# Optimization experiments

Hardware: AMD Instinct MI355X
Metric: run time of the kernel (lower is better)

## Reference

```python
import jax, jax.numpy as jnp
import numpy as np

N, D, H = 4096, 1024, 8
HD = D // H
FFN = int(D * 1.5)
TAU_NEG = 0.6
BETA = 1.5
LN_EPS = 1e-5


def _layernorm(x, g, b):
    mu = jnp.mean(x, axis=-1, keepdims=True)
    var = jnp.mean((x - mu) ** 2, axis=-1, keepdims=True)
    return (x - mu) * jax.lax.rsqrt(var + LN_EPS) * g + b


def setup_inputs() -> dict:
    key = jax.random.key(0)
    ks = jax.random.split(key, 16)
    s = 0.02
    inp = {
        "features": jax.random.normal(ks[0], (N, D), jnp.float32),
        "coords": jax.random.randint(ks[1], (N, 2), 0, 128, jnp.int32),
        "Wq": jax.random.normal(ks[2], (D, D), jnp.float32) * s,
        "Wk": jax.random.normal(ks[3], (D, D), jnp.float32) * s,
        "Wv": jax.random.normal(ks[4], (D, D), jnp.float32) * s,
        "Wo": jax.random.normal(ks[5], (D, D), jnp.float32) * s,
        "bo": jnp.zeros((D,), jnp.float32),
        "ln1_g": jnp.ones((D,), jnp.float32),
        "ln1_b": jnp.zeros((D,), jnp.float32),
        "W1": jax.random.normal(ks[6], (FFN, D), jnp.float32) * s,
        "b1": jnp.zeros((FFN,), jnp.float32),
        "W2": jax.random.normal(ks[7], (D, FFN), jnp.float32) * s,
        "b2": jnp.zeros((D,), jnp.float32),
        "ln2_g": jnp.ones((D,), jnp.float32),
        "ln2_b": jnp.zeros((D,), jnp.float32),
    }
    return inp


def reference(features, coords, Wq, Wk, Wv, Wo, bo, ln1_g, ln1_b, W1, b1, W2, b2, ln2_g, ln2_b):
    # QKV projections (torch Linear: x @ W.T), reshape to [H, N, HD]
    Q = (features @ Wq.T).reshape(N, H, HD).transpose(1, 0, 2)
    K = (features @ Wk.T).reshape(N, H, HD).transpose(1, 0, 2)
    V = (features @ Wv.T).reshape(N, H, HD).transpose(1, 0, 2)

    scores = jnp.einsum('hnd,hmd->hnm', Q, K) / jnp.sqrt(jnp.float32(HD))  # [H,N,N]

    # spatial distance bias from barcode coords, scaled per head by 1/2^(h+1)
    c = coords.astype(jnp.float32)
    diff = c[:, None, :] - c[None, :, :]
    dist = jnp.sqrt(jnp.sum(diff ** 2, axis=-1))  # [N,N]
    head_scalings = 1.0 / (2.0 ** (jnp.arange(1, H + 1, dtype=jnp.float32)))
    bias = dist[None, :, :] * head_scalings[:, None, None]  # [H,N,N]

    attn_pos = jax.nn.softmax(scores - bias, axis=-1)
    attn_neg = jax.nn.softmax((-scores - bias) / TAU_NEG, axis=-1)
    attn = attn_pos - BETA * attn_neg  # dropout is identity in eval

    attended = jnp.einsum('hnm,hmd->hnd', attn, V)  # [H,N,HD]
    attended = attended.transpose(1, 0, 2).reshape(N, D)

    x = attended @ Wo.T + bo + features
    x = _layernorm(x, ln1_g, ln1_b)

    h = jax.nn.gelu(x @ W1.T + b1, approximate=False)  # torch default GELU = exact erf
    ffn_out = h @ W2.T + b2
    return _layernorm(ffn_out + x, ln2_g, ln2_b)
```

## Files before the change

kernel.cpp:

```cpp
#include <hip/hip_runtime.h>
#include <cstdint>
#include <cstddef>

#define NTOK 4096
#define DMODEL 1024
#define NHEAD 8
#define DHEAD 128
#define DFFN 1536
#define LNEPS 1e-5f

typedef __bf16 bf16_t;
typedef __bf16 bf16x8 __attribute__((ext_vector_type(8)));
typedef __bf16 bf16x4 __attribute__((ext_vector_type(4)));
typedef float f32x4 __attribute__((ext_vector_type(4)));
typedef float f32x16 __attribute__((ext_vector_type(16)));

__device__ __forceinline__ void gload_lds16(const bf16_t* g, bf16_t* lds) {
  __builtin_amdgcn_global_load_lds(
      (const __attribute__((address_space(1))) unsigned int*)g,
      (__attribute__((address_space(3))) unsigned int*)lds, 16, 0, 0);
}

__device__ __forceinline__ float fexp2(float x) {
  float r;
  asm("v_exp_f32 %0, %1" : "=v"(r) : "v"(x));
  return r;
}
__device__ __forceinline__ float fsqrt(float x) {
  float r;
  asm("v_sqrt_f32 %0, %1" : "=v"(r) : "v"(x));
  return r;
}
__device__ __forceinline__ unsigned cvtpk(float lo, float hi) {
  unsigned r;
  asm("v_cvt_pk_bf16_f32 %0, %1, %2" : "=v"(r) : "v"(lo), "v"(hi));
  return r;
}

#define CVT_TOTAL 2885632
__global__ __launch_bounds__(256) void cvt_all(
    const float* __restrict__ f, const float* __restrict__ wq,
    const float* __restrict__ wk, const float* __restrict__ wv,
    const float* __restrict__ wo, const float* __restrict__ w1,
    const float* __restrict__ w2, const int* __restrict__ coords,
    bf16_t* __restrict__ fb, bf16_t* __restrict__ wqkv,
    bf16_t* __restrict__ wob, bf16_t* __restrict__ w1b,
    bf16_t* __restrict__ w2b, float2* __restrict__ cfl)
{
  for (int u = blockIdx.x * 256 + threadIdx.x; u < CVT_TOTAL; u += 2048 * 256) {
    if (u < 2048) {
      int4 c = reinterpret_cast<const int4*>(coords)[u];
      float4 o;
      o.x = (float)c.x; o.y = (float)c.y; o.z = (float)c.z; o.w = (float)c.w;
      reinterpret_cast<float4*>(cfl)[u] = o;
      continue;
    }
    int v = u - 2048;
    const float* src; bf16_t* dst; int base;
    if (v < 1048576)      { src = f;  dst = fb;            base = 0; }
    else if (v < 1310720) { src = wq; dst = wqkv;          base = 1048576; }
    else if (v < 1572864) { src = wk; dst = wqkv + 1048576; base = 1310720; }
    else if (v < 1835008) { src = wv; dst = wqkv + 2097152; base = 1572864; }
    else if (v < 2097152) { src = wo; dst = wob;           base = 1835008; }
    else if (v < 2490368) { src = w1; dst = w1b;           base = 2097152; }
    else                  { src = w2; dst = w2b;           base = 2490368; }
    int local = v - base;
    const float4 x = reinterpret_cast<const float4*>(src)[local];
    bf16x4 o = {(bf16_t)x.x, (bf16_t)x.y, (bf16_t)x.z, (bf16_t)x.w};
    reinterpret_cast<bf16x4*>(dst)[local] = o;
  }
}

template<int EPI>
__global__ __launch_bounds__(256) void gemm_bt(
    const bf16_t* __restrict__ A, const bf16_t* __restrict__ B,
    int M, int Nn, int K,
    const float* __restrict__ bias, const float* __restrict__ resid,
    const bf16_t* __restrict__ residH,
    float* __restrict__ outF, bf16_t* __restrict__ outH)
{
  __shared__ bf16_t As[2][64 * 32];
  __shared__ bf16_t Bs[2][128 * 32];
  const int t = threadIdx.x;
  const int w = t >> 6, l = t & 63;
  const int lg = l >> 4, li = l & 15;
  const int m0 = blockIdx.x * 64, n0 = blockIdx.y * 128;
  const int wr = (w >> 1) * 32, wc = (w & 1) * 64;
  const f32x4 fz = {0.f, 0.f, 0.f, 0.f};
  f32x4 acc[2][4];
#pragma unroll
  for (int i = 0; i < 2; i++)
#pragma unroll
    for (int j = 0; j < 4; j++) acc[i][j] = fz;

  const bf16_t* Ag = A + (size_t)m0 * K;
  const bf16_t* Bg = B + (size_t)n0 * K;
  const int ca = w * 64 + l;
  const int nK = K >> 5;

  gload_lds16(Ag + (size_t)(ca >> 2) * K + (ca & 3) * 8, &As[0][(w * 64) * 8]);
#pragma unroll
  for (int p = 0; p < 2; p++) {
    int cb = p * 256 + ca;
    gload_lds16(Bg + (size_t)(cb >> 2) * K + (cb & 3) * 8, &Bs[0][(p * 256 + w * 64) * 8]);
  }
  __syncthreads();

  for (int ki = 0; ki < nK; ki++) {
    const int cur = ki & 1;
    if (ki + 1 < nK) {
      const int kt = (ki + 1) << 5;
      gload_lds16(Ag + (size_t)(ca >> 2) * K + kt + (ca & 3) * 8,
                  &As[cur ^ 1][(w * 64) * 8]);
#pragma unroll
      for (int p = 0; p < 2; p++) {
        int cb = p * 256 + ca;
        gload_lds16(Bg + (size_t)(cb >> 2) * K + kt + (cb & 3) * 8,
                    &Bs[cur ^ 1][(p * 256 + w * 64) * 8]);
      }
    }
    bf16x8 af[2], bfr[4];
#pragma unroll
    for (int mi = 0; mi < 2; mi++)
      af[mi] = *reinterpret_cast<const bf16x8*>(&As[cur][(wr + mi * 16 + li) * 32 + lg * 8]);
#pragma unroll
    for (int ni = 0; ni < 4; ni++)
      bfr[ni] = *reinterpret_cast<const bf16x8*>(&Bs[cur][(wc + ni * 16 + li) * 32 + lg * 8]);
#pragma unroll
    for (int mi = 0; mi < 2; mi++)
#pragma unroll
      for (int ni = 0; ni < 4; ni++)
        acc[mi][ni] = __builtin_amdgcn_mfma_f32_16x16x32_bf16(af[mi], bfr[ni], acc[mi][ni], 0, 0, 0);
    __syncthreads();
  }

#pragma unroll
  for (int mi = 0; mi < 2; mi++) {
#pragma unroll
    for (int ni = 0; ni < 4; ni++) {
      int gcol = n0 + wc + ni * 16 + li;
#pragma unroll
      for (int r = 0; r < 4; r++) {
        int grow = m0 + wr + mi * 16 + lg * 4 + r;
        float v = acc[mi][ni][r];
        if (EPI == 0) {
          outH[(size_t)grow * Nn + gcol] = (bf16_t)v;
        } else if (EPI == 1) {
          v += bias[gcol] + resid[(size_t)grow * Nn + gcol];
          outF[(size_t)grow * Nn + gcol] = v;
        } else if (EPI == 2) {
          v += bias[gcol];
          v = 0.5f * v * (1.f + erff(v * 0.70710678118654752f));
          outH[(size_t)grow * Nn + gcol] = (bf16_t)v;
        } else {
          v += bias[gcol] + (float)residH[(size_t)grow * Nn + gcol];
          outF[(size_t)grow * Nn + gcol] = v;
        }
      }
    }
  }
}

__global__ __launch_bounds__(256) void gemm_qkv(
    const bf16_t* __restrict__ A, const bf16_t* __restrict__ B,
    bf16_t* __restrict__ Qo, bf16_t* __restrict__ Kp, bf16_t* __restrict__ Vp)
{
  const int K = DMODEL;
  __shared__ bf16_t As[2][64 * 32];
  __shared__ bf16_t Bs[2][128 * 32];
  const int t = threadIdx.x;
  const int w = t >> 6, l = t & 63;
  const int lg = l >> 4, li = l & 15;
  const int m0 = blockIdx.x * 64, n0 = blockIdx.y * 128;
  const int wr = (w >> 1) * 32, wc = (w & 1) * 64;
  const f32x4 fz = {0.f, 0.f, 0.f, 0.f};
  f32x4 acc[2][4];
#pragma unroll
  for (int i = 0; i < 2; i++)
#pragma unroll
    for (int j = 0; j < 4; j++) acc[i][j] = fz;

  const bf16_t* Ag = A + (size_t)m0 * K;
  const bf16_t* Bg = B + (size_t)n0 * K;
  const int ca = w * 64 + l;
  const int nK = K >> 5;

  gload_lds16(Ag + (size_t)(ca >> 2) * K + (ca & 3) * 8, &As[0][(w * 64) * 8]);
#pragma unroll
  for (int p = 0; p < 2; p++) {
    int cb = p * 256 + ca;
    gload_lds16(Bg + (size_t)(cb >> 2) * K + (cb & 3) * 8, &Bs[0][(p * 256 + w * 64) * 8]);
  }
  __syncthreads();

  for (int ki = 0; ki < nK; ki++) {
    const int cur = ki & 1;
    if (ki + 1 < nK) {
      const int kt = (ki + 1) << 5;
      gload_lds16(Ag + (size_t)(ca >> 2) * K + kt + (ca & 3) * 8,
                  &As[cur ^ 1][(w * 64) * 8]);
#pragma unroll
      for (int p = 0; p < 2; p++) {
        int cb = p * 256 + ca;
        gload_lds16(Bg + (size_t)(cb >> 2) * K + kt + (cb & 3) * 8,
                    &Bs[cur ^ 1][(p * 256 + w * 64) * 8]);
      }
    }
    bf16x8 af[2], bfr[4];
#pragma unroll
    for (int mi = 0; mi < 2; mi++)
      af[mi] = *reinterpret_cast<const bf16x8*>(&As[cur][(wr + mi * 16 + li) * 32 + lg * 8]);
#pragma unroll
    for (int ni = 0; ni < 4; ni++)
      bfr[ni] = *reinterpret_cast<const bf16x8*>(&Bs[cur][(wc + ni * 16 + li) * 32 + lg * 8]);
#pragma unroll
    for (int mi = 0; mi < 2; mi++)
#pragma unroll
      for (int ni = 0; ni < 4; ni++)
        acc[mi][ni] = __builtin_amdgcn_mfma_f32_16x16x32_bf16(af[mi], bfr[ni], acc[mi][ni], 0, 0, 0);
    __syncthreads();
  }

  const int region = n0 >> 10;
#pragma unroll
  for (int mi = 0; mi < 2; mi++) {
#pragma unroll
    for (int ni = 0; ni < 4; ni++) {
      int gcol = n0 + wc + ni * 16 + li;
#pragma unroll
      for (int r = 0; r < 4; r++) {
        int token = m0 + wr + mi * 16 + lg * 4 + r;
        bf16_t v = (bf16_t)acc[mi][ni][r];
        if (region == 0) {
          Qo[(size_t)token * DMODEL + gcol] = v;
        } else if (region == 1) {
          int gc = gcol - 1024;
          int h = gc >> 7, d = gc & 127;
          size_t addr = ((size_t)(h * 128 + (token >> 5))) * 4096 +
                        (d >> 4) * 512 + ((d >> 3) & 1) * 256 + (token & 31) * 8 + (d & 7);
          Kp[addr] = v;
        } else {
          int gc = gcol - 2048;
          int h = gc >> 7, dh = gc & 127;
          size_t addr = ((size_t)(h * 128 + (token >> 5))) * 4096 +
                        (((token >> 4) & 1) * 4 + (dh >> 5)) * 512 +
                        ((token >> 3) & 1) * 256 + (dh & 31) * 8 + (token & 7);
          Vp[addr] = v;
        }
      }
    }
  }
}

__global__ __launch_bounds__(128, 2) void attn9_kernel(
    const bf16_t* __restrict__ Q, const bf16_t* __restrict__ Kp,
    const bf16_t* __restrict__ Vp, const float2* __restrict__ cf,
    bf16_t* __restrict__ out)
{
  __shared__ float buf[128 * 33];
  __shared__ float mlS[2][32];

  const int t = threadIdx.x;
  const int w = t >> 6;
  const int l = t & 63;
  const int q5 = l & 31;
  const int hi = l >> 5;
  const int h = blockIdx.x & 7;
  const int q0 = (blockIdx.x >> 3) * 32;
  const float LOG2E = 1.44269504088896f;
  const float isq = 0.08838834764831845f;
  const float itau = 1.6666666666666667f;
  const float hs = 1.0f / (float)(2 << h);
  const float ap = isq * LOG2E;
  const float an = -isq * itau * LOG2E;
  const float bpp = hs * LOG2E;

  bf16x8 qf[8];
  {
    const bf16_t* qrow = Q + (size_t)(q0 + q5) * DMODEL + h * DHEAD;
#pragma unroll
    for (int c = 0; c < 8; c++)
      qf[c] = *reinterpret_cast<const bf16x8*>(qrow + c * 16 + hi * 8);
  }
  const float2 qc = cf[q0 + q5];
  const float qxs = qc.x * bpp, qys = qc.y * bpp;

  f32x16 accp[4], accn[4];
#pragma unroll
  for (int f = 0; f < 4; f++) {
#pragma unroll
    for (int r = 0; r < 16; r++) { accp[f][r] = 0.f; accn[f][r] = 0.f; }
  }
  float lp = 0.f, lN = 0.f;

  const bf16_t* kpb = Kp + ((size_t)(h * 128 + w * 64)) * 4096 + l * 8;
  const bf16_t* vpb = Vp + ((size_t)(h * 128 + w * 64)) * 4096 + l * 8;

  for (int it = 0; it < 64; it++) {
    const int kv0 = w * 2048 + it * 32;

    bf16x8 kf[8];
#pragma unroll
    for (int c = 0; c < 8; c++)
      kf[c] = *reinterpret_cast<const bf16x8*>(kpb + (size_t)it * 4096 + c * 512);

    f32x16 sacc, sacc2;
#pragma unroll
    for (int r = 0; r < 16; r++) { sacc[r] = 0.f; sacc2[r] = 0.f; }
#pragma unroll
    for (int c = 0; c < 4; c++) {
      sacc = __builtin_amdgcn_mfma_f32_32x32x16_bf16(kf[2 * c], qf[2 * c], sacc, 0, 0, 0);
      sacc2 = __builtin_amdgcn_mfma_f32_32x32x16_bf16(kf[2 * c + 1], qf[2 * c + 1], sacc2, 0, 0, 0);
    }

    bf16x8 vf[8];
#pragma unroll
    for (int fr = 0; fr < 8; fr++)
      vf[fr] = *reinterpret_cast<const bf16x8*>(vpb + (size_t)it * 4096 + fr * 512);

#pragma unroll
    for (int r = 0; r < 16; r++) sacc[r] += sacc2[r];

    float p16[16], n16[16];
#pragma unroll
    for (int r = 0; r < 16; r++) {
      int kvr = kv0 + (r & 3) + 8 * (r >> 2) + 4 * hi;
      float2 c = cf[kvr];
      float dx = __builtin_fmaf(c.x, -bpp, qxs);
      float dy = __builtin_fmaf(c.y, -bpp, qys);
      float u = fsqrt(__builtin_fmaf(dy, dy, dx * dx));
      float pv = fexp2(__builtin_fmaf(sacc[r], ap, -u));
      float nv = fexp2(__builtin_fmaf(sacc[r], an, u * -itau));
      p16[r] = pv; n16[r] = nv;
      lp += pv; lN += nv;
    }

    unsigned pw[2][4], nw[2][4];
#pragma unroll
    for (int ks = 0; ks < 2; ks++) {
#pragma unroll
      for (int u = 0; u < 2; u++) {
        unsigned A = cvtpk(p16[8 * ks + 2 * u], p16[8 * ks + 2 * u + 1]);
        unsigned B = cvtpk(p16[8 * ks + 4 + 2 * u], p16[8 * ks + 4 + 2 * u + 1]);
        unsigned Ax = __shfl_xor(A, 32, 64);
        unsigned Bx = __shfl_xor(B, 32, 64);
        pw[ks][u] = hi ? Bx : A;
        pw[ks][2 + u] = hi ? B : Ax;
        unsigned C = cvtpk(n16[8 * ks + 2 * u], n16[8 * ks + 2 * u + 1]);
        unsigned D = cvtpk(n16[8 * ks + 4 + 2 * u], n16[8 * ks + 4 + 2 * u + 1]);
        unsigned Cx = __shfl_xor(C, 32, 64);
        unsigned Dx = __shfl_xor(D, 32, 64);
        nw[ks][u] = hi ? Dx : C;
        nw[ks][2 + u] = hi ? D : Cx;
      }
    }

#pragma unroll
    for (int ks = 0; ks < 2; ks++) {
      union { unsigned u[4]; bf16x8 v; } pb, nb;
#pragma unroll
      for (int j = 0; j < 4; j++) { pb.u[j] = pw[ks][j]; nb.u[j] = nw[ks][j]; }
#pragma unroll
      for (int f = 0; f < 4; f++) {
        accp[f] = __builtin_amdgcn_mfma_f32_32x32x16_bf16(vf[ks * 4 + f], pb.v, accp[f], 0, 0, 0);
        accn[f] = __builtin_amdgcn_mfma_f32_32x32x16_bf16(vf[ks * 4 + f], nb.v, accn[f], 0, 0, 0);
      }
    }
  }

  float lpw = lp + __shfl_xor(lp, 32, 64);
  float lnw = lN + __shfl_xor(lN, 32, 64);

  __syncthreads();
  if (w == 1) {
    if (hi == 0) { mlS[0][q5] = lpw; mlS[1][q5] = lnw; }
#pragma unroll
    for (int f = 0; f < 4; f++)
#pragma unroll
      for (int r = 0; r < 16; r++)
        buf[(32 * f + (r & 3) + 8 * (r >> 2) + 4 * hi) * 33 + q5] = accp[f][r];
  }
  __syncthreads();
  float lpt = 0.f, lnt = 0.f;
  if (w == 0) {
    lpt = lpw + mlS[0][q5];
    lnt = lnw + mlS[1][q5];
#pragma unroll
    for (int f = 0; f < 4; f++)
#pragma unroll
      for (int r = 0; r < 16; r++)
        accp[f][r] += buf[(32 * f + (r & 3) + 8 * (r >> 2) + 4 * hi) * 33 + q5];
  }
  __syncthreads();
  if (w == 1) {
#pragma unroll
    for (int f = 0; f < 4; f++)
#pragma unroll
      for (int r = 0; r < 16; r++)
        buf[(32 * f + (r & 3) + 8 * (r >> 2) + 4 * hi) * 33 + q5] = accn[f][r];
  }
  __syncthreads();
  if (w == 0) {
    float ip = 1.f / lpt, inn = 1.5f / lnt;
#pragma unroll
    for (int f = 0; f < 4; f++)
#pragma unroll
      for (int r = 0; r < 16; r++) {
        int row = 32 * f + (r & 3) + 8 * (r >> 2) + 4 * hi;
        float an2 = accn[f][r] + buf[row * 33 + q5];
        buf[row * 33 + q5] = accp[f][r] * ip - an2 * inn;
      }
  }
  __syncthreads();

  {
    int q = t >> 2, dq = (t & 3) * 32;
#pragma unroll
    for (int j = 0; j < 4; j++) {
      bf16x8 ov;
#pragma unroll
      for (int e = 0; e < 8; e++) ov[e] = (bf16_t)buf[(dq + j * 8 + e) * 33 + q];
      *reinterpret_cast<bf16x8*>(out + (size_t)(q0 + q) * DMODEL + h * DHEAD + dq + j * 8) = ov;
    }
  }
}

__global__ __launch_bounds__(256) void ln_kernel(
    const float* __restrict__ in, const float* __restrict__ g, const float* __restrict__ b,
    float* __restrict__ outF, bf16_t* __restrict__ outH)
{
  int row = blockIdx.x, t = threadIdx.x;
  const float4 v = reinterpret_cast<const float4*>(in + (size_t)row * DMODEL)[t];
  float s = v.x + v.y + v.z + v.w;
  float ss = v.x * v.x + v.y * v.y + v.z * v.z + v.w * v.w;
#pragma unroll
  for (int m = 32; m >= 1; m >>= 1) {
    s += __shfl_xor(s, m, 64);
    ss += __shfl_xor(ss, m, 64);
  }
  __shared__ float red[8];
  int w = t >> 6, l = t & 63;
  if (l == 0) { red[w] = s; red[4 + w] = ss; }
  __syncthreads();
  s = red[0] + red[1] + red[2] + red[3];
  ss = red[4] + red[5] + red[6] + red[7];
  float mu = s * (1.f / DMODEL);
  float var = ss * (1.f / DMODEL) - mu * mu;
  float rs = rsqrtf(var + LNEPS);
  const float4 gv = reinterpret_cast<const float4*>(g)[t];
  const float4 bv = reinterpret_cast<const float4*>(b)[t];
  float y0 = (v.x - mu) * rs * gv.x + bv.x;
  float y1 = (v.y - mu) * rs * gv.y + bv.y;
  float y2 = (v.z - mu) * rs * gv.z + bv.z;
  float y3 = (v.w - mu) * rs * gv.w + bv.w;
  if (outF) {
    float4 o; o.x = y0; o.y = y1; o.z = y2; o.w = y3;
    reinterpret_cast<float4*>(outF + (size_t)row * DMODEL)[t] = o;
  }
  if (outH) {
    bf16x4 o = {(bf16_t)y0, (bf16_t)y1, (bf16_t)y2, (bf16_t)y3};
    reinterpret_cast<bf16x4*>(outH + (size_t)row * DMODEL)[t] = o;
  }
}

extern "C" void kernel_launch(void* const* d_in, const int* in_sizes, int n_in,
                              void* d_out, int out_size, void* d_ws, size_t ws_size,
                              hipStream_t stream) {
  (void)in_sizes; (void)n_in; (void)out_size; (void)ws_size;
  const float* features = (const float*)d_in[0];
  const int* coords = (const int*)d_in[1];
  const float* Wq = (const float*)d_in[2];
  const float* Wk = (const float*)d_in[3];
  const float* Wv = (const float*)d_in[4];
  const float* Wo = (const float*)d_in[5];
  const float* bo = (const float*)d_in[6];
  const float* ln1g = (const float*)d_in[7];
  const float* ln1b = (const float*)d_in[8];
  const float* W1 = (const float*)d_in[9];
  const float* b1 = (const float*)d_in[10];
  const float* W2 = (const float*)d_in[11];
  const float* b2 = (const float*)d_in[12];
  const float* ln2g = (const float*)d_in[13];
  const float* ln2b = (const float*)d_in[14];
  float* outp = (float*)d_out;

  char* ws = (char*)d_ws;
  size_t off = 0;
  auto alloc = [&](size_t bytes) -> void* {
    void* p = ws + off;
    off += (bytes + 255) & ~((size_t)255);
    return p;
  };
  bf16_t* fb16 = (bf16_t*)alloc((size_t)NTOK * DMODEL * 2);
  bf16_t* wqkv16 = (bf16_t*)alloc((size_t)3 * DMODEL * DMODEL * 2);
  bf16_t* wo16 = (bf16_t*)alloc((size_t)DMODEL * DMODEL * 2);
  bf16_t* w116 = (bf16_t*)alloc((size_t)DFFN * DMODEL * 2);
  bf16_t* w216 = (bf16_t*)alloc((size_t)DMODEL * DFFN * 2);
  bf16_t* q16 = (bf16_t*)alloc((size_t)NTOK * DMODEL * 2);
  bf16_t* Kp = (bf16_t*)alloc((size_t)NTOK * DMODEL * 2);
  bf16_t* Vp = (bf16_t*)alloc((size_t)NTOK * DMODEL * 2);
  float* acc1 = (float*)alloc((size_t)NTOK * DMODEL * 4);
  bf16_t* x16 = (bf16_t*)alloc((size_t)NTOK * DMODEL * 2);
  bf16_t* h16 = (bf16_t*)alloc((size_t)NTOK * DFFN * 2);
  float2* cfl = (float2*)alloc((size_t)NTOK * sizeof(float2));
  bf16_t* att16 = fb16;

  cvt_all<<<dim3(2048), 256, 0, stream>>>(features, Wq, Wk, Wv, Wo, W1, W2, coords,
                                          fb16, wqkv16, wo16, w116, w216, cfl);

  gemm_qkv<<<dim3(NTOK / 64, 3 * DMODEL / 128), 256, 0, stream>>>(fb16, wqkv16, q16, Kp, Vp);
  attn9_kernel<<<dim3(NTOK / 32 * NHEAD), 128, 0, stream>>>(q16, Kp, Vp, cfl, att16);
  dim3 gO(NTOK / 64, DMODEL / 128);
  gemm_bt<1><<<gO, 256, 0, stream>>>(att16, wo16, NTOK, DMODEL, DMODEL, bo, features, nullptr, acc1, nullptr);
  ln_kernel<<<dim3(NTOK), 256, 0, stream>>>(acc1, ln1g, ln1b, nullptr, x16);
  gemm_bt<2><<<dim3(NTOK / 64, DFFN / 128), 256, 0, stream>>>(x16, w116, NTOK, DFFN, DMODEL, b1, nullptr, nullptr, nullptr, h16);
  gemm_bt<3><<<gO, 256, 0, stream>>>(h16, w216, NTOK, DMODEL, DFFN, b2, nullptr, x16, acc1, nullptr);
  ln_kernel<<<dim3(NTOK), 256, 0, stream>>>(acc1, ln2g, ln2b, outp, nullptr);
}
```

Measured before the change: 313.4 us.

## Enlarge QKV GEMM tile, use permlane32 swap and MFMA priority in attention

After: 314.6 us. About the same (+0.4%).

```diff
diff --git a/kernel.cpp b/kernel.cpp
--- a/kernel.cpp
+++ b/kernel.cpp
@@ -166,30 +166,29 @@
     bf16_t* __restrict__ Qo, bf16_t* __restrict__ Kp, bf16_t* __restrict__ Vp)
 {
   const int K = DMODEL;
-  __shared__ bf16_t As[2][64 * 32];
+  __shared__ bf16_t As[2][128 * 32];
   __shared__ bf16_t Bs[2][128 * 32];
   const int t = threadIdx.x;
   const int w = t >> 6, l = t & 63;
   const int lg = l >> 4, li = l & 15;
-  const int m0 = blockIdx.x * 64, n0 = blockIdx.y * 128;
-  const int wr = (w >> 1) * 32, wc = (w & 1) * 64;
+  const int m0 = blockIdx.x * 128, n0 = blockIdx.y * 128;
+  const int wr = (w >> 1) * 64, wc = (w & 1) * 64;
   const f32x4 fz = {0.f, 0.f, 0.f, 0.f};
-  f32x4 acc[2][4];
-#pragma unroll
-  for (int i = 0; i < 2; i++)
+  f32x4 acc[4][4];
+#pragma unroll
+  for (int i = 0; i < 4; i++)
 #pragma unroll
     for (int j = 0; j < 4; j++) acc[i][j] = fz;
 
   const bf16_t* Ag = A + (size_t)m0 * K;
   const bf16_t* Bg = B + (size_t)n0 * K;
-  const int ca = w * 64 + l;
   const int nK = K >> 5;
 
-  gload_lds16(Ag + (size_t)(ca >> 2) * K + (ca & 3) * 8, &As[0][(w * 64) * 8]);
 #pragma unroll
   for (int p = 0; p < 2; p++) {
-    int cb = p * 256 + ca;
-    gload_lds16(Bg + (size_t)(cb >> 2) * K + (cb & 3) * 8, &Bs[0][(p * 256 + w * 64) * 8]);
+    int c = p * 256 + w * 64 + l;
+    gload_lds16(Ag + (size_t)(c >> 2) * K + (c & 3) * 8, &As[0][(p * 256 + w * 64) * 8]);
+    gload_lds16(Bg + (size_t)(c >> 2) * K + (c & 3) * 8, &Bs[0][(p * 256 + w * 64) * 8]);
   }
   __syncthreads();
 
@@ -197,24 +196,24 @@
     const int cur = ki & 1;
     if (ki + 1 < nK) {
       const int kt = (ki + 1) << 5;
-      gload_lds16(Ag + (size_t)(ca >> 2) * K + kt + (ca & 3) * 8,
-                  &As[cur ^ 1][(w * 64) * 8]);
 #pragma unroll
       for (int p = 0; p < 2; p++) {
-        int cb = p * 256 + ca;
-        gload_lds16(Bg + (size_t)(cb >> 2) * K + kt + (cb & 3) * 8,
+        int c = p * 256 + w * 64 + l;
+        gload_lds16(Ag + (size_t)(c >> 2) * K + kt + (c & 3) * 8,
+                    &As[cur ^ 1][(p * 256 + w * 64) * 8]);
+        gload_lds16(Bg + (size_t)(c >> 2) * K + kt + (c & 3) * 8,
                     &Bs[cur ^ 1][(p * 256 + w * 64) * 8]);
       }
     }
-    bf16x8 af[2], bfr[4];
-#pragma unroll
-    for (int mi = 0; mi < 2; mi++)
+    bf16x8 af[4], bfr[4];
+#pragma unroll
+    for (int mi = 0; mi < 4; mi++)
       af[mi] = *reinterpret_cast<const bf16x8*>(&As[cur][(wr + mi * 16 + li) * 32 + lg * 8]);
 #pragma unroll
     for (int ni = 0; ni < 4; ni++)
       bfr[ni] = *reinterpret_cast<const bf16x8*>(&Bs[cur][(wc + ni * 16 + li) * 32 + lg * 8]);
 #pragma unroll
-    for (int mi = 0; mi < 2; mi++)
+    for (int mi = 0; mi < 4; mi++)
 #pragma unroll
       for (int ni = 0; ni < 4; ni++)
         acc[mi][ni] = __builtin_amdgcn_mfma_f32_16x16x32_bf16(af[mi], bfr[ni], acc[mi][ni], 0, 0, 0);
@@ -223,7 +222,7 @@
 
   const int region = n0 >> 10;
 #pragma unroll
-  for (int mi = 0; mi < 2; mi++) {
+  for (int mi = 0; mi < 4; mi++) {
 #pragma unroll
     for (int ni = 0; ni < 4; ni++) {
       int gcol = n0 + wc + ni * 16 + li;
@@ -252,7 +251,7 @@
   }
 }
 
-__global__ __launch_bounds__(128, 2) void attn9_kernel(
+__global__ __launch_bounds__(128, 2) void attn10_kernel(
     const bf16_t* __restrict__ Q, const bf16_t* __restrict__ Kp,
     const bf16_t* __restrict__ Vp, const float2* __restrict__ cf,
     bf16_t* __restrict__ out)
@@ -307,11 +306,13 @@
     f32x16 sacc, sacc2;
 #pragma unroll
     for (int r = 0; r < 16; r++) { sacc[r] = 0.f; sacc2[r] = 0.f; }
+    __builtin_amdgcn_s_setprio(1);
 #pragma unroll
     for (int c = 0; c < 4; c++) {
       sacc = __builtin_amdgcn_mfma_f32_32x32x16_bf16(kf[2 * c], qf[2 * c], sacc, 0, 0, 0);
       sacc2 = __builtin_amdgcn_mfma_f32_32x32x16_bf16(kf[2 * c + 1], qf[2 * c + 1], sacc2, 0, 0, 0);
     }
+    __builtin_amdgcn_s_setprio(0);
 
     bf16x8 vf[8];
 #pragma unroll
@@ -342,19 +343,18 @@
       for (int u = 0; u < 2; u++) {
         unsigned A = cvtpk(p16[8 * ks + 2 * u], p16[8 * ks + 2 * u + 1]);
         unsigned B = cvtpk(p16[8 * ks + 4 + 2 * u], p16[8 * ks + 4 + 2 * u + 1]);
-        unsigned Ax = __shfl_xor(A, 32, 64);
-        unsigned Bx = __shfl_xor(B, 32, 64);
-        pw[ks][u] = hi ? Bx : A;
-        pw[ks][2 + u] = hi ? B : Ax;
+        asm("v_permlane32_swap_b32 %0, %1" : "+v"(A), "+v"(B));
+        pw[ks][u] = A;
+        pw[ks][2 + u] = B;
         unsigned C = cvtpk(n16[8 * ks + 2 * u], n16[8 * ks + 2 * u + 1]);
         unsigned D = cvtpk(n16[8 * ks + 4 + 2 * u], n16[8 * ks + 4 + 2 * u + 1]);
-        unsigned Cx = __shfl_xor(C, 32, 64);
-        unsigned Dx = __shfl_xor(D, 32, 64);
-        nw[ks][u] = hi ? Dx : C;
-        nw[ks][2 + u] = hi ? D : Cx;
-      }
-    }
-
+        asm("v_permlane32_swap_b32 %0, %1" : "+v"(C), "+v"(D));
+        nw[ks][u] = C;
+        nw[ks][2 + u] = D;
+      }
+    }
+
+    __builtin_amdgcn_s_setprio(1);
 #pragma unroll
     for (int ks = 0; ks < 2; ks++) {
       union { unsigned u[4]; bf16x8 v; } pb, nb;
@@ -366,6 +366,7 @@
         accn[f] = __builtin_amdgcn_mfma_f32_32x32x16_bf16(vf[ks * 4 + f], nb.v, accn[f], 0, 0, 0);
       }
     }
+    __builtin_amdgcn_s_setprio(0);
   }
 
   float lpw = lp + __shfl_xor(lp, 32, 64);
@@ -508,8 +509,8 @@
   cvt_all<<<dim3(2048), 256, 0, stream>>>(features, Wq, Wk, Wv, Wo, W1, W2, coords,
                                           fb16, wqkv16, wo16, w116, w216, cfl);
 
-  gemm_qkv<<<dim3(NTOK / 64, 3 * DMODEL / 128), 256, 0, stream>>>(fb16, wqkv16, q16, Kp, Vp);
-  attn9_kernel<<<dim3(NTOK / 32 * NHEAD), 128, 0, stream>>>(q16, Kp, Vp, cfl, att16);
+  gemm_qkv<<<dim3(NTOK / 128, 3 * DMODEL / 128), 256, 0, stream>>>(fb16, wqkv16, q16, Kp, Vp);
+  attn10_kernel<<<dim3(NTOK / 32 * NHEAD), 128, 0, stream>>>(q16, Kp, Vp, cfl, att16);
   dim3 gO(NTOK / 64, DMODEL / 128);
   gemm_bt<1><<<gO, 256, 0, stream>>>(att16, wo16, NTOK, DMODEL, DMODEL, bo, features, nullptr, acc1, nullptr);
   ln_kernel<<<dim3(NTOK), 256, 0, stream>>>(acc1, ln1g, ln1b, nullptr, x16);
```
